# Performance work log

Measured on AMD Instinct MI355X. Metric: run time of the kernel, lower is better.

Reference implementation:

```python
import jax, jax.numpy as jnp
import numpy as np

S = 64        # FARGAN_SUBFRAME_SIZE
NSUB = 4      # FARGAN_SUBFRAMES
HOP = 256     # HOPSIZE = NSUB * S
NF = 256      # num_features
GC = 256      # global_channels
IC = NF + GC  # input_channels
B = 64
T = 100

NOISE_KEY = jax.random.key(1)


def _w(k, shape):
    return jax.random.normal(k, shape, dtype=jnp.float32) / np.sqrt(shape[-1]).astype(np.float32)


def setup_inputs() -> dict:
    key = jax.random.key(0)
    ks = jax.random.split(key, 20)
    return {
        'features': jax.random.normal(ks[0], (B, NF, T), dtype=jnp.float32),
        'global_features': jax.random.normal(ks[1], (B, GC, 1), dtype=jnp.float32),
        'in_W1': _w(ks[2], (IC, IC)),
        'in_b1': jnp.zeros((IC,), jnp.float32),
        'in_W2': _w(ks[3], (HOP, IC)),
        'in_b2': jnp.zeros((HOP,), jnp.float32),
        'fw_W': _w(ks[4], (S, 2 * S)),
        'fw_glu_W': _w(ks[5], (S, S)),
        'gru1_Wih': _w(ks[6], (3 * S, 2 * S)),
        'gru1_Whh': _w(ks[7], (3 * S, S)),
        'glu1_W': _w(ks[8], (S, S)),
        'gru2_Wih': _w(ks[9], (3 * S, 2 * S)),
        'gru2_Whh': _w(ks[10], (3 * S, S)),
        'glu2_W': _w(ks[11], (S, S)),
        'gru3_Wih': _w(ks[12], (3 * S, 2 * S)),
        'gru3_Whh': _w(ks[13], (3 * S, S)),
        'glu3_W': _w(ks[14], (S, S)),
        'skip_dense_W': _w(ks[15], (2 * S, 5 * S)),
        'skip_glu_W': _w(ks[16], (2 * S, 2 * S)),
        'out_W': _w(ks[17], (S, 2 * S)),
    }


def _noise(x, k):
    return jnp.clip(x + (jax.random.uniform(k, x.shape, x.dtype) - 0.5) * (1.0 / 127.0), -1.0, 1.0)


def _glu(x, W):
    return x * jax.nn.sigmoid(x @ W.T)


def _gru_cell(x, h, Wih, Whh):
    gi = x @ Wih.T  # [B, 3S]
    gh = h @ Whh.T
    i_r, i_z, i_n = jnp.split(gi, 3, axis=-1)
    h_r, h_z, h_n = jnp.split(gh, 3, axis=-1)
    r = jax.nn.sigmoid(i_r + h_r)
    z = jax.nn.sigmoid(i_z + h_z)
    n = jnp.tanh(i_n + r * h_n)
    return (1.0 - z) * n + z * h


def _forward(features, global_features, in_W1, in_b1, in_W2, in_b2, fw_W, fw_glu_W,
             gru1_Wih, gru1_Whh, glu1_W, gru2_Wih, gru2_Whh, glu2_W,
             gru3_Wih, gru3_Whh, glu3_W, skip_dense_W, skip_glu_W, out_W):
    b = features.shape[0]
    t = features.shape[2]
    g = global_features[:, :, 0]  # [B, GC]

    def subframe_step(sub, prev, st, key):
        h1, h2, h3, s3 = st
        kk = jax.random.split(key, 10)
        sub = _noise(sub, kk[0])
        prev = _noise(prev, kk[1])
        fw = _noise(_glu(jnp.tanh(jnp.concatenate([sub, s3], -1) @ fw_W.T), fw_glu_W), kk[2])
        h1n = _gru_cell(jnp.concatenate([fw, prev], -1), h1, gru1_Wih, gru1_Whh)
        g1 = _noise(_glu(_noise(h1n, kk[3]), glu1_W), kk[4])
        h2n = _gru_cell(jnp.concatenate([g1, prev], -1), h2, gru2_Wih, gru2_Whh)
        g2 = _noise(_glu(_noise(h2n, kk[5]), glu2_W), kk[6])
        h3n = _gru_cell(jnp.concatenate([g2, prev], -1), h3, gru3_Wih, gru3_Whh)
        g3 = _noise(_glu(_noise(h3n, kk[7]), glu3_W), kk[8])
        skip_feats = jnp.concatenate([g1, g2, g3, fw, prev], -1)  # [B, 5S]
        skip = _glu(_noise(jnp.tanh(skip_feats @ skip_dense_W.T), kk[9]), skip_glu_W)
        out = jnp.tanh(skip @ out_W.T)  # [B, S]
        return out, (h1n, h2n, h3n, sub)

    def frame_step(carry, f_t):
        st, prev, i = carry
        x = jnp.tanh(jnp.concatenate([f_t, g], -1) @ in_W1.T + in_b1) @ in_W2.T + in_b2  # [B, HOP]
        outs = []
        for s in range(NSUB):
            k = jax.random.fold_in(NOISE_KEY, i * NSUB + s)
            o, st = subframe_step(x[:, s * S:(s + 1) * S], prev, st, k)
            prev = o
            outs.append(o)
        return (st, prev, i + 1), jnp.concatenate(outs, -1)

    z = jnp.zeros((b, S), features.dtype)
    init = ((z, z, z, z), z, jnp.int32(0))
    xs = jnp.transpose(features, (2, 0, 1))  # [T, B, NF]
    _, ys = jax.lax.scan(frame_step, init, xs)  # [T, B, HOP]
    signal = jnp.transpose(ys, (1, 0, 2)).reshape(b, t * HOP)
    return signal[:, None, :]  # [B, 1, T*HOP]


def reference(features, global_features, in_W1, in_b1, in_W2, in_b2, fw_W, fw_glu_W,
              gru1_Wih, gru1_Whh, glu1_W, gru2_Wih, gru2_Whh, glu2_W,
              gru3_Wih, gru3_Whh, glu3_W, skip_dense_W, skip_glu_W, out_W):
    return _forward(features, global_features, in_W1, in_b1, in_W2, in_b2, fw_W, fw_glu_W,
                    gru1_Wih, gru1_Whh, glu1_W, gru2_Wih, gru2_Whh, glu2_W,
                    gru3_Wih, gru3_Whh, glu3_W, skip_dense_W, skip_glu_W, out_W)
```

## Files before the change

### kernel.cpp

```cpp
#include <hip/hip_runtime.h>
#include <stdint.h>

#define SS 64
#define BB 64
#define TT 100
#define HOPC 256
#define NFC 256
#define GCC 256
#define ICC 512
#define NC (1.0f/127.0f)
#define NBLK 64
#define NTHR 512

#define OFF_FW     0
#define OFF_FWGLU  8192
#define OFF_G1IH   12288
#define OFF_G1HH   36864
#define OFF_GLU1   49152
#define OFF_G2IH   53248
#define OFF_G2HH   77824
#define OFF_GLU2   90112
#define OFF_G3IH   94208
#define OFF_G3HH   118784
#define OFF_GLU3   131072
#define OFF_SKIPD  135168
#define OFF_SKIPG  176128
#define OFF_OUT    192512
#define W_TOTAL    200704
#define XALL_F32   (TT * BB * HOPC)

typedef _Float16 f16;
typedef _Float16 h2 __attribute__((ext_vector_type(2)));
union U16 { uint4 u; h2 h[4]; };

#if __has_builtin(__builtin_amdgcn_fdot2)
#define FDOT2(a, b, c) __builtin_amdgcn_fdot2((a), (b), (c), false)
#else
#define FDOT2(a, b, c) ((c) + (float)(a)[0] * (float)(b)[0] + (float)(a)[1] * (float)(b)[1])
#endif

__device__ __forceinline__ uint32_t rotl32(uint32_t x, int r) {
    return (x << r) | (x >> (32 - r));
}

__device__ __forceinline__ void tf2x32(uint32_t k0, uint32_t k1, uint32_t c0, uint32_t c1,
                                       uint32_t& o0, uint32_t& o1) {
    uint32_t k2 = k0 ^ k1 ^ 0x1BD11BDAu;
    uint32_t x0 = c0 + k0, x1 = c1 + k1;
    x0 += x1; x1 = rotl32(x1, 13); x1 ^= x0;
    x0 += x1; x1 = rotl32(x1, 15); x1 ^= x0;
    x0 += x1; x1 = rotl32(x1, 26); x1 ^= x0;
    x0 += x1; x1 = rotl32(x1, 6);  x1 ^= x0;
    x0 += k1; x1 += k2 + 1u;
    x0 += x1; x1 = rotl32(x1, 17); x1 ^= x0;
    x0 += x1; x1 = rotl32(x1, 29); x1 ^= x0;
    x0 += x1; x1 = rotl32(x1, 16); x1 ^= x0;
    x0 += x1; x1 = rotl32(x1, 24); x1 ^= x0;
    x0 += k2; x1 += k0 + 2u;
    x0 += x1; x1 = rotl32(x1, 13); x1 ^= x0;
    x0 += x1; x1 = rotl32(x1, 15); x1 ^= x0;
    x0 += x1; x1 = rotl32(x1, 26); x1 ^= x0;
    x0 += x1; x1 = rotl32(x1, 6);  x1 ^= x0;
    x0 += k0; x1 += k1 + 3u;
    x0 += x1; x1 = rotl32(x1, 17); x1 ^= x0;
    x0 += x1; x1 = rotl32(x1, 29); x1 ^= x0;
    x0 += x1; x1 = rotl32(x1, 16); x1 ^= x0;
    x0 += x1; x1 = rotl32(x1, 24); x1 ^= x0;
    x0 += k1; x1 += k2 + 4u;
    x0 += x1; x1 = rotl32(x1, 13); x1 ^= x0;
    x0 += x1; x1 = rotl32(x1, 15); x1 ^= x0;
    x0 += x1; x1 = rotl32(x1, 26); x1 ^= x0;
    x0 += x1; x1 = rotl32(x1, 6);  x1 ^= x0;
    x0 += k2; x1 += k0 + 5u;
    o0 = x0; o1 = x1;
}

__device__ __forceinline__ float unifP(uint32_t k0, uint32_t k1, uint32_t m) {
    uint32_t o0, o1;
    tf2x32(k0, k1, 0u, m, o0, o1);
    uint32_t bits = o0 ^ o1;
    return __uint_as_float((bits >> 9) | 0x3f800000u) - 1.0f;
}

__device__ __forceinline__ float clipf(float v) { return fminf(1.0f, fmaxf(-1.0f, v)); }
__device__ __forceinline__ float noiseu(float v, float u) {
    return clipf(v + (u - 0.5f) * NC);
}
__device__ __forceinline__ float sigmf(float v) {
    return __fdividef(1.0f, 1.0f + __expf(-v));
}
__device__ __forceinline__ float tanhfast(float x) {
    float ax = fminf(fabsf(x), 15.0f);
    float e = __expf(2.0f * ax);
    float r = __fdividef(e - 1.0f, e + 1.0f);
    return copysignf(r, x);
}

__device__ __forceinline__ float red8dpp(float v) {
    int t;
    t = __builtin_amdgcn_update_dpp(0, __float_as_int(v), 0xB1, 0xF, 0xF, true);
    v += __int_as_float(t);
    t = __builtin_amdgcn_update_dpp(0, __float_as_int(v), 0x4E, 0xF, 0xF, true);
    v += __int_as_float(t);
    t = __builtin_amdgcn_update_dpp(0, __float_as_int(v), 0x141, 0xF, 0xF, true);
    v += __int_as_float(t);
    return v;
}

__device__ __forceinline__ float dotU(const U16& w, const U16& x, float acc) {
#pragma unroll
    for (int i = 0; i < 4; ++i) acc = FDOT2(w.h[i], x.h[i], acc);
    return acc;
}

struct WF1  { U16 w[2]; };
struct WGRU { U16 wih[6]; U16 whh[3]; U16 glu; };
struct WSK  { U16 w[10]; };
struct WSG  { U16 w[4]; };

__device__ __forceinline__ void ldF1(const f16* W, int row, int g, WF1& r) {
    const f16* p = W + row * 128 + g * 16;
    r.w[0].u = *(const uint4*)p;
    r.w[1].u = *(const uint4*)(p + 8);
}
__device__ __forceinline__ void ldF2(const f16* W, int row, int g, U16& r) {
    r.u = *(const uint4*)(W + row * 64 + g * 8);
}
__device__ __forceinline__ void ldGRU(const f16* Wih, const f16* Whh, const f16* Glu,
                                      int row, int g, WGRU& r) {
#pragma unroll
    for (int j = 0; j < 3; ++j) {
        const f16* p = Wih + (row + 64 * j) * 128 + g * 16;
        r.wih[2 * j].u     = *(const uint4*)p;
        r.wih[2 * j + 1].u = *(const uint4*)(p + 8);
        r.whh[j].u = *(const uint4*)(Whh + (row + 64 * j) * 64 + g * 8);
    }
    r.glu.u = *(const uint4*)(Glu + row * 64 + g * 8);
}
__device__ __forceinline__ void ldSK(const f16* W, int row, int g, WSK& r) {
#pragma unroll
    for (int j = 0; j < 2; ++j) {
        const f16* p = W + (row + 64 * j) * 320 + g * 40;
#pragma unroll
        for (int i = 0; i < 5; ++i) r.w[5 * j + i].u = *(const uint4*)(p + 8 * i);
    }
}
__device__ __forceinline__ void ldSG(const f16* W, int row, int g, WSG& r) {
#pragma unroll
    for (int j = 0; j < 2; ++j) {
        const f16* p = W + (row + 64 * j) * 128 + g * 16;
        r.w[2 * j].u     = *(const uint4*)p;
        r.w[2 * j + 1].u = *(const uint4*)(p + 8);
    }
}

__device__ __forceinline__ void pinU(U16& r) {
    asm volatile("" : "+v"(r.u.x), "+v"(r.u.y), "+v"(r.u.z), "+v"(r.u.w));
}

struct SrcW { const float* p[14]; };

__global__ __launch_bounds__(256) void fargan_cvtw(SrcW s, f16* __restrict__ dst) {
    const int offs[15] = {0, 8192, 12288, 36864, 49152, 53248, 77824, 90112,
                          94208, 118784, 131072, 135168, 176128, 192512, 200704};
    int i = blockIdx.x * 256 + threadIdx.x;
    if (i >= W_TOTAL) return;
    int sgi = 0;
#pragma unroll
    for (int t = 1; t < 14; ++t) sgi += (i >= offs[t]);
    dst[i] = (f16)s.p[sgi][i - offs[sgi]];
}

__global__ __launch_bounds__(256) void fargan_tr(const float* __restrict__ f,
                                                 float* __restrict__ fT) {
    __shared__ float L[64][104];
    int b = blockIdx.x >> 2, c0 = (blockIdx.x & 3) * 64;
    for (int e = threadIdx.x; e < 6400; e += 256) {
        int r = e / 100, col = e - r * 100;
        L[r][col] = f[b * NFC * TT + (c0 + r) * TT + col];
    }
    __syncthreads();
    for (int e = threadIdx.x; e < 6400; e += 256) {
        int t = e >> 6, c = e & 63;
        fT[(t * BB + b) * NFC + c0 + c] = L[c][t];
    }
}

__global__ __launch_bounds__(256) void fargan_frame(
    const float* __restrict__ fT, const float* __restrict__ gfeat,
    const float* __restrict__ W1, const float* __restrict__ ib1,
    const float* __restrict__ W2, const float* __restrict__ ib2,
    float* __restrict__ xall)
{
    __shared__ __align__(16) float cat[16][ICC];
    __shared__ __align__(16) float zb[16][ICC];
    const int tid = threadIdx.x;
    const int t = blockIdx.x >> 2;
    const int q = blockIdx.x & 3;

    for (int bb = 0; bb < 16; ++bb) {
        int b = q * 16 + bb;
        for (int c = tid; c < ICC; c += 256) {
            float v = (c < NFC) ? fT[(t * BB + b) * NFC + c]
                                : gfeat[b * GCC + (c - NFC)];
            cat[bb][c] = v;
        }
    }
    __syncthreads();

    {
        int rg = tid & 63, bg = tid >> 6;
        int n0 = rg * 8, bb0 = bg * 4;
        float acc[8][4];
#pragma unroll
        for (int r = 0; r < 8; ++r)
#pragma unroll
            for (int j = 0; j < 4; ++j) acc[r][j] = 0.f;
        for (int k = 0; k < ICC; k += 4) {
            float4 cv[4];
#pragma unroll
            for (int j = 0; j < 4; ++j) cv[j] = *(const float4*)&cat[bb0 + j][k];
#pragma unroll
            for (int r = 0; r < 8; ++r) {
                float4 wv = *(const float4*)&W1[(n0 + r) * ICC + k];
#pragma unroll
                for (int j = 0; j < 4; ++j)
                    acc[r][j] += wv.x * cv[j].x + wv.y * cv[j].y + wv.z * cv[j].z + wv.w * cv[j].w;
            }
        }
#pragma unroll
        for (int r = 0; r < 8; ++r) {
            float bias = ib1[n0 + r];
#pragma unroll
            for (int j = 0; j < 4; ++j)
                zb[bb0 + j][n0 + r] = tanhf(acc[r][j] + bias);
        }
    }
    __syncthreads();

    {
        int rg = tid & 63, bg = tid >> 6;
        int n0 = rg * 4, bb0 = bg * 4;
        float acc[4][4];
#pragma unroll
        for (int r = 0; r < 4; ++r)
#pragma unroll
            for (int j = 0; j < 4; ++j) acc[r][j] = 0.f;
        for (int k = 0; k < ICC; k += 4) {
            float4 cv[4];
#pragma unroll
            for (int j = 0; j < 4; ++j) cv[j] = *(const float4*)&zb[bb0 + j][k];
#pragma unroll
            for (int r = 0; r < 4; ++r) {
                float4 wv = *(const float4*)&W2[(n0 + r) * ICC + k];
#pragma unroll
                for (int j = 0; j < 4; ++j)
                    acc[r][j] += wv.x * cv[j].x + wv.y * cv[j].y + wv.z * cv[j].z + wv.w * cv[j].w;
            }
        }
#pragma unroll
        for (int r = 0; r < 4; ++r) {
            float bias = ib2[n0 + r];
#pragma unroll
            for (int j = 0; j < 4; ++j) {
                int b = q * 16 + bb0 + j;
                xall[(t * BB + b) * HOPC + n0 + r] = acc[r][j] + bias;
            }
        }
    }
}

__global__ __launch_bounds__(512, 2) void fargan_seq(
    const float* __restrict__ xall, const f16* __restrict__ wh,
    float* __restrict__ outp)
{
    const int tid = threadIdx.x;
    const int row = tid >> 3;
    const int g = tid & 7;
    const int bg = blockIdx.x;

    __shared__ __align__(16) f16 XH[128];
    __shared__ __align__(16) f16 SKXH[320];
    __shared__ __align__(16) f16 TWH[64], HNH[64];
    __shared__ __align__(16) f16 SPNH[128], SKVH[128];
    __shared__ __align__(16) f16 HH[2][3][64];
    __shared__ __align__(16) float Hf[2][3][64];
    __shared__ __align__(16) float UNF[704];
    __shared__ uint32_t kkb[2][20];

    WF1 rF1;  ldF1(wh + OFF_FW, row, g, rF1);
    U16 rF2;  ldF2(wh + OFF_FWGLU, row, g, rF2);
    WGRU rG1; ldGRU(wh + OFF_G1IH, wh + OFF_G1HH, wh + OFF_GLU1, row, g, rG1);
    WGRU rG2; ldGRU(wh + OFF_G2IH, wh + OFF_G2HH, wh + OFF_GLU2, row, g, rG2);
    WGRU rG3; ldGRU(wh + OFF_G3IH, wh + OFF_G3HH, wh + OFF_GLU3, row, g, rG3);
    WSG rSG;  ldSG(wh + OFF_SKIPG, row, g, rSG);
    WF1 rOUT; ldF1(wh + OFF_OUT, row, g, rOUT);

    pinU(rF1.w[0]); pinU(rF1.w[1]); pinU(rF2);
#pragma unroll
    for (int j = 0; j < 6; ++j) { pinU(rG1.wih[j]); pinU(rG2.wih[j]); pinU(rG3.wih[j]); }
#pragma unroll
    for (int j = 0; j < 3; ++j) { pinU(rG1.whh[j]); pinU(rG2.whh[j]); pinU(rG3.whh[j]); }
    pinU(rG1.glu); pinU(rG2.glu); pinU(rG3.glu);
#pragma unroll
    for (int j = 0; j < 4; ++j) pinU(rSG.w[j]);
    pinU(rOUT.w[0]); pinU(rOUT.w[1]);

    float prevO = 0.f, xs_old = 0.f;
    if (g == 0) {
#pragma unroll
        for (int i = 0; i < 3; ++i) { Hf[0][i][row] = 0.f; HH[0][i][row] = (f16)0.f; }
        XH[row] = (f16)0.f; XH[64 + row] = (f16)0.f;
    }
    if (tid < 10) {
        uint32_t f0, f1; tf2x32(0u, 1u, 0u, 0u, f0, f1);
        uint32_t A, Bv;  tf2x32(f0, f1, 0u, (uint32_t)tid, A, Bv);
        kkb[0][2 * tid] = A; kkb[0][2 * tid + 1] = Bv;
    }
    __syncthreads();

    for (int t = 0; t < TT; ++t) {
        for (int s = 0; s < 4; ++s) {
            const int idx = t * 4 + s;
            const int p = idx & 1;

            float xv = xall[(t * BB + bg) * HOPC + s * SS + row];
            if (g == 0) {
                const uint32_t m64 = (uint32_t)(bg * 64 + row);
                float u0 = unifP(kkb[p][0], kkb[p][1], m64);
                float u1 = unifP(kkb[p][2], kkb[p][3], m64);
                float xs = noiseu(xv, u0);
                XH[row] = (f16)xs; XH[64 + row] = (f16)xs_old; xs_old = xs;
                SKXH[256 + row] = (f16)noiseu(prevO, u1);
            } else {
                int wid = row * 7 + g - 1;
                int j = 128 + wid;
                int sl = j >> 6;
                UNF[j] = unifP(kkb[p][2 * sl], kkb[p][2 * sl + 1],
                               (uint32_t)(bg * 64 + (j & 63)));
                if (wid < 128)
                    UNF[576 + wid] = unifP(kkb[p][18], kkb[p][19],
                                           (uint32_t)(bg * 128 + wid));
            }
            if (g == 7 && row >= 54) {
                int i = row - 54;
                uint32_t f0, f1; tf2x32(0u, 1u, 0u, (uint32_t)(idx + 1), f0, f1);
                uint32_t A, Bv;  tf2x32(f0, f1, 0u, (uint32_t)i, A, Bv);
                kkb[p ^ 1][2 * i] = A; kkb[p ^ 1][2 * i + 1] = Bv;
            }
            __syncthreads();

            float twv;
            {
                U16 xa, xb;
                xa.u = *(const uint4*)&XH[g * 16];
                xb.u = *(const uint4*)&XH[g * 16 + 8];
                float a = dotU(rF1.w[0], xa, 0.f);
                a = dotU(rF1.w[1], xb, a);
                twv = tanhfast(red8dpp(a));
                if (g == 0) TWH[row] = (f16)twv;
            }
            __syncthreads();

            {
                U16 xa; xa.u = *(const uint4*)&TWH[g * 8];
                float a = red8dpp(dotU(rF2, xa, 0.f));
                if (g == 0) SKXH[192 + row] = (f16)noiseu(twv * sigmf(a), UNF[128 + row]);
            }
            __syncthreads();

#define GRU_STEP(RG, XPTR, GI, UH, UG, GOFF)                                               \
            {                                                                               \
                const f16* xin = (XPTR);                                                    \
                U16 xa, xb, xh;                                                             \
                xa.u = *(const uint4*)xin;                                                  \
                xb.u = *(const uint4*)(xin + 8);                                            \
                xh.u = *(const uint4*)&HH[p][GI][g * 8];                                    \
                float ai0 = 0, ai1 = 0, ai2 = 0, ah0 = 0, ah1 = 0, ah2 = 0;                 \
                ai0 = dotU(RG.wih[0], xa, ai0); ai0 = dotU(RG.wih[1], xb, ai0);             \
                ai1 = dotU(RG.wih[2], xa, ai1); ai1 = dotU(RG.wih[3], xb, ai1);             \
                ai2 = dotU(RG.wih[4], xa, ai2); ai2 = dotU(RG.wih[5], xb, ai2);             \
                ah0 = dotU(RG.whh[0], xh, ah0);                                             \
                ah1 = dotU(RG.whh[1], xh, ah1);                                             \
                ah2 = dotU(RG.whh[2], xh, ah2);                                             \
                ai0 = red8dpp(ai0); ai1 = red8dpp(ai1); ai2 = red8dpp(ai2);                 \
                ah0 = red8dpp(ah0); ah1 = red8dpp(ah1); ah2 = red8dpp(ah2);                 \
                float hold = Hf[p][GI][row];                                                \
                float r  = sigmf(ai0 + ah0);                                                \
                float z  = sigmf(ai1 + ah1);                                                \
                float nn = tanhfast(ai2 + r * ah2);                                         \
                float hnew = (1.f - z) * nn + z * hold;                                     \
                float hNv = noiseu(hnew, UNF[(UH) + row]);                                  \
                if (g == 0) {                                                               \
                    Hf[p ^ 1][GI][row] = hnew;                                              \
                    HH[p ^ 1][GI][row] = (f16)hnew;                                         \
                    HNH[row] = (f16)hNv;                                                    \
                }                                                                           \
                __syncthreads();                                                            \
                U16 xg; xg.u = *(const uint4*)&HNH[g * 8];                                  \
                float ag = red8dpp(dotU(RG.glu, xg, 0.f));                                  \
                if (g == 0) SKXH[(GOFF) + row] =                                            \
                    (f16)noiseu(hNv * sigmf(ag), UNF[(UG) + row]);                          \
            }                                                                               \
            __syncthreads();

            GRU_STEP(rG1, SKXH + 192 + g * 16, 0, 192, 256, 0)
            GRU_STEP(rG2, (g < 4 ? SKXH + g * 16 : SKXH + 256 + (g - 4) * 16), 1, 320, 384, 64)
            WSK rSK; ldSK(wh + OFF_SKIPD, row, g, rSK);
            GRU_STEP(rG3, (g < 4 ? SKXH + 64 + g * 16 : SKXH + 256 + (g - 4) * 16), 2, 448, 512, 128)
#undef GRU_STEP

            float sp0, sp1;
            {
                U16 xs[5];
#pragma unroll
                for (int i = 0; i < 5; ++i) xs[i].u = *(const uint4*)&SKXH[g * 40 + 8 * i];
                float a0 = 0, a1 = 0;
#pragma unroll
                for (int i = 0; i < 5; ++i) {
                    a0 = dotU(rSK.w[i], xs[i], a0);
                    a1 = dotU(rSK.w[5 + i], xs[i], a1);
                }
                sp0 = noiseu(tanhfast(red8dpp(a0)), UNF[576 + row]);
                sp1 = noiseu(tanhfast(red8dpp(a1)), UNF[640 + row]);
                if (g == 0) { SPNH[row] = (f16)sp0; SPNH[64 + row] = (f16)sp1; }
            }
            __syncthreads();

            {
                U16 xa, xb;
                xa.u = *(const uint4*)&SPNH[g * 16];
                xb.u = *(const uint4*)&SPNH[g * 16 + 8];
                float a0 = dotU(rSG.w[0], xa, 0.f); a0 = dotU(rSG.w[1], xb, a0);
                float a1 = dotU(rSG.w[2], xa, 0.f); a1 = dotU(rSG.w[3], xb, a1);
                a0 = red8dpp(a0); a1 = red8dpp(a1);
                if (g == 0) {
                    SKVH[row]      = (f16)(sp0 * sigmf(a0));
                    SKVH[64 + row] = (f16)(sp1 * sigmf(a1));
                }
            }
            __syncthreads();

            {
                U16 xa, xb;
                xa.u = *(const uint4*)&SKVH[g * 16];
                xb.u = *(const uint4*)&SKVH[g * 16 + 8];
                float a = dotU(rOUT.w[0], xa, 0.f);
                a = dotU(rOUT.w[1], xb, a);
                float o = tanhfast(red8dpp(a));
                prevO = o;
                if (g == 0) outp[bg * (TT * HOPC) + t * HOPC + s * SS + row] = o;
            }
        }
    }
}

extern "C" void kernel_launch(void* const* d_in, const int* in_sizes, int n_in,
                              void* d_out, int out_size, void* d_ws, size_t ws_size,
                              hipStream_t stream) {
    const float* features = (const float*)d_in[0];
    const float* gfeat    = (const float*)d_in[1];
    const float* W1       = (const float*)d_in[2];
    const float* ib1      = (const float*)d_in[3];
    const float* W2       = (const float*)d_in[4];
    const float* ib2      = (const float*)d_in[5];

    float* xall = (float*)d_ws;
    float* fT   = xall + XALL_F32;
    f16*   wh   = (f16*)(fT + XALL_F32);
    float* outp = (float*)d_out;

    SrcW sw;
    for (int i = 0; i < 14; ++i) sw.p[i] = (const float*)d_in[6 + i];

    hipLaunchKernelGGL(fargan_cvtw, dim3((W_TOTAL + 255) / 256), dim3(256), 0, stream, sw, wh);
    hipLaunchKernelGGL(fargan_tr, dim3(256), dim3(256), 0, stream, features, fT);
    hipLaunchKernelGGL(fargan_frame, dim3(TT * 4), dim3(256), 0, stream,
                       fT, gfeat, W1, ib1, W2, ib2, xall);
    hipLaunchKernelGGL(fargan_seq, dim3(NBLK), dim3(NTHR), 0, stream, xall, wh, outp);
}
```

Measured before the change: 2.834 ms.

## Precompute RNG keys, double-buffer noise generation, prefetch inputs, lighten barriers

All 401 per-subframe Threefry keys are computed once at kernel start into a shared table, so the serial per-step key derivation is gone. Uniform noise for the next subframe is generated into a double-buffered array, with the work split across the idle slots of several stages. Next-frame input values are prefetched into registers a frame ahead. __syncthreads is replaced by an inline-asm LDS wait plus s_barrier, which skips waiting on global memory; this relies on no cross-thread dependence through global memory and uses more shared memory.

```diff
diff --git a/kernel.cpp b/kernel.cpp
--- a/kernel.cpp
+++ b/kernel.cpp
@@ -96,6 +96,10 @@
     return copysignf(r, x);
 }
 
+__device__ __forceinline__ void bar_lds() {
+    asm volatile("s_waitcnt lgkmcnt(0)\n\ts_barrier" ::: "memory");
+}
+
 __device__ __forceinline__ float red8dpp(float v) {
     int t;
     t = __builtin_amdgcn_update_dpp(0, __float_as_int(v), 0xB1, 0xF, 0xF, true);
@@ -285,8 +289,8 @@
     __shared__ __align__(16) f16 SPNH[128], SKVH[128];
     __shared__ __align__(16) f16 HH[2][3][64];
     __shared__ __align__(16) float Hf[2][3][64];
-    __shared__ __align__(16) float UNF[704];
-    __shared__ uint32_t kkb[2][20];
+    __shared__ __align__(16) float UNF[2][704];
+    __shared__ uint32_t KK[401][20];
 
     WF1 rF1;  ldF1(wh + OFF_FW, row, g, rF1);
     U16 rF2;  ldF2(wh + OFF_FWGLU, row, g, rF2);
@@ -312,43 +316,49 @@
         for (int i = 0; i < 3; ++i) { Hf[0][i][row] = 0.f; HH[0][i][row] = (f16)0.f; }
         XH[row] = (f16)0.f; XH[64 + row] = (f16)0.f;
     }
-    if (tid < 10) {
-        uint32_t f0, f1; tf2x32(0u, 1u, 0u, 0u, f0, f1);
-        uint32_t A, Bv;  tf2x32(f0, f1, 0u, (uint32_t)tid, A, Bv);
-        kkb[0][2 * tid] = A; kkb[0][2 * tid + 1] = Bv;
+
+    for (int e = tid; e < 4010; e += NTHR) {
+        int ii = e / 10, ki = e - ii * 10;
+        uint32_t f0, f1; tf2x32(0u, 1u, 0u, (uint32_t)ii, f0, f1);
+        uint32_t A, Bv;  tf2x32(f0, f1, 0u, (uint32_t)ki, A, Bv);
+        KK[ii][2 * ki] = A; KK[ii][2 * ki + 1] = Bv;
     }
     __syncthreads();
 
+    for (int j = tid; j < 704; j += NTHR) {
+        int sl = j >> 6;
+        int kx = (sl < 9) ? 2 * sl : 18;
+        uint32_t m = (sl < 9) ? (uint32_t)(bg * 64 + (j & 63))
+                              : (uint32_t)(bg * 128 + (j - 576));
+        UNF[0][j] = unifP(KK[0][kx], KK[0][kx + 1], m);
+    }
+
+    float xf0 = xall[(0 * BB + bg) * HOPC + 0 * SS + row];
+    float xf1 = xall[(0 * BB + bg) * HOPC + 1 * SS + row];
+    float xf2 = xall[(0 * BB + bg) * HOPC + 2 * SS + row];
+    float xf3 = xall[(0 * BB + bg) * HOPC + 3 * SS + row];
+    __syncthreads();
+
     for (int t = 0; t < TT; ++t) {
+        const int tn = (t + 1 < TT) ? t + 1 : t;
+        float xn0 = xall[(tn * BB + bg) * HOPC + 0 * SS + row];
+        float xn1 = xall[(tn * BB + bg) * HOPC + 1 * SS + row];
+        float xn2 = xall[(tn * BB + bg) * HOPC + 2 * SS + row];
+        float xn3 = xall[(tn * BB + bg) * HOPC + 3 * SS + row];
+
         for (int s = 0; s < 4; ++s) {
             const int idx = t * 4 + s;
             const int p = idx & 1;
 
-            float xv = xall[(t * BB + bg) * HOPC + s * SS + row];
             if (g == 0) {
-                const uint32_t m64 = (uint32_t)(bg * 64 + row);
-                float u0 = unifP(kkb[p][0], kkb[p][1], m64);
-                float u1 = unifP(kkb[p][2], kkb[p][3], m64);
+                float u0 = UNF[p][row];
+                float u1 = UNF[p][64 + row];
+                float xv = (s == 0) ? xf0 : (s == 1) ? xf1 : (s == 2) ? xf2 : xf3;
                 float xs = noiseu(xv, u0);
                 XH[row] = (f16)xs; XH[64 + row] = (f16)xs_old; xs_old = xs;
                 SKXH[256 + row] = (f16)noiseu(prevO, u1);
-            } else {
-                int wid = row * 7 + g - 1;
-                int j = 128 + wid;
-                int sl = j >> 6;
-                UNF[j] = unifP(kkb[p][2 * sl], kkb[p][2 * sl + 1],
-                               (uint32_t)(bg * 64 + (j & 63)));
-                if (wid < 128)
-                    UNF[576 + wid] = unifP(kkb[p][18], kkb[p][19],
-                                           (uint32_t)(bg * 128 + wid));
-            }
-            if (g == 7 && row >= 54) {
-                int i = row - 54;
-                uint32_t f0, f1; tf2x32(0u, 1u, 0u, (uint32_t)(idx + 1), f0, f1);
-                uint32_t A, Bv;  tf2x32(f0, f1, 0u, (uint32_t)i, A, Bv);
-                kkb[p ^ 1][2 * i] = A; kkb[p ^ 1][2 * i + 1] = Bv;
-            }
-            __syncthreads();
+            }
+            bar_lds();
 
             float twv;
             {
@@ -360,22 +370,28 @@
                 twv = tanhfast(red8dpp(a));
                 if (g == 0) TWH[row] = (f16)twv;
             }
-            __syncthreads();
+            bar_lds();
 
             {
                 U16 xa; xa.u = *(const uint4*)&TWH[g * 8];
+                if (tid < 256) {
+                    int kx = 2 * (tid >> 6);
+                    UNF[p ^ 1][tid] = unifP(KK[idx + 1][kx], KK[idx + 1][kx + 1],
+                                            (uint32_t)(bg * 64 + (tid & 63)));
+                }
                 float a = red8dpp(dotU(rF2, xa, 0.f));
-                if (g == 0) SKXH[192 + row] = (f16)noiseu(twv * sigmf(a), UNF[128 + row]);
-            }
-            __syncthreads();
-
-#define GRU_STEP(RG, XPTR, GI, UH, UG, GOFF)                                               \
+                if (g == 0) SKXH[192 + row] = (f16)noiseu(twv * sigmf(a), UNF[p][128 + row]);
+            }
+            bar_lds();
+
+#define GRU_STEP(RG, XPTR, GI, UH, UG, GOFF, EXTRA)                                         \
             {                                                                               \
                 const f16* xin = (XPTR);                                                    \
                 U16 xa, xb, xh;                                                             \
                 xa.u = *(const uint4*)xin;                                                  \
                 xb.u = *(const uint4*)(xin + 8);                                            \
                 xh.u = *(const uint4*)&HH[p][GI][g * 8];                                    \
+                EXTRA;                                                                      \
                 float ai0 = 0, ai1 = 0, ai2 = 0, ah0 = 0, ah1 = 0, ah2 = 0;                 \
                 ai0 = dotU(RG.wih[0], xa, ai0); ai0 = dotU(RG.wih[1], xb, ai0);             \
                 ai1 = dotU(RG.wih[2], xa, ai1); ai1 = dotU(RG.wih[3], xb, ai1);             \
@@ -390,25 +406,37 @@
                 float z  = sigmf(ai1 + ah1);                                                \
                 float nn = tanhfast(ai2 + r * ah2);                                         \
                 float hnew = (1.f - z) * nn + z * hold;                                     \
-                float hNv = noiseu(hnew, UNF[(UH) + row]);                                  \
+                float hNv = noiseu(hnew, UNF[p][(UH) + row]);                               \
                 if (g == 0) {                                                               \
                     Hf[p ^ 1][GI][row] = hnew;                                              \
                     HH[p ^ 1][GI][row] = (f16)hnew;                                         \
                     HNH[row] = (f16)hNv;                                                    \
                 }                                                                           \
-                __syncthreads();                                                            \
+                bar_lds();                                                                  \
                 U16 xg; xg.u = *(const uint4*)&HNH[g * 8];                                  \
                 float ag = red8dpp(dotU(RG.glu, xg, 0.f));                                  \
                 if (g == 0) SKXH[(GOFF) + row] =                                            \
-                    (f16)noiseu(hNv * sigmf(ag), UNF[(UG) + row]);                          \
+                    (f16)noiseu(hNv * sigmf(ag), UNF[p][(UG) + row]);                       \
             }                                                                               \
-            __syncthreads();
-
-            GRU_STEP(rG1, SKXH + 192 + g * 16, 0, 192, 256, 0)
-            GRU_STEP(rG2, (g < 4 ? SKXH + g * 16 : SKXH + 256 + (g - 4) * 16), 1, 320, 384, 64)
+            bar_lds();
+
+#define NOISE_A2 do { if (tid >= 256) {                                                     \
+                int kx = 2 * (tid >> 6);                                                    \
+                UNF[p ^ 1][tid] = unifP(KK[idx + 1][kx], KK[idx + 1][kx + 1],               \
+                                        (uint32_t)(bg * 64 + (tid & 63))); } } while (0)
+#define NOISE_B do { int j2 = tid + 512; if (j2 < 704) {                                    \
+                int kx = (j2 < 576) ? 16 : 18;                                              \
+                uint32_t m2 = (j2 < 576) ? (uint32_t)(bg * 64 + (j2 & 63))                  \
+                                         : (uint32_t)(bg * 128 + (j2 - 576));               \
+                UNF[p ^ 1][j2] = unifP(KK[idx + 1][kx], KK[idx + 1][kx + 1], m2); } } while (0)
+
+            GRU_STEP(rG1, SKXH + 192 + g * 16, 0, 192, 256, 0, NOISE_A2)
+            GRU_STEP(rG2, (g < 4 ? SKXH + g * 16 : SKXH + 256 + (g - 4) * 16), 1, 320, 384, 64, NOISE_B)
             WSK rSK; ldSK(wh + OFF_SKIPD, row, g, rSK);
-            GRU_STEP(rG3, (g < 4 ? SKXH + 64 + g * 16 : SKXH + 256 + (g - 4) * 16), 2, 448, 512, 128)
+            GRU_STEP(rG3, (g < 4 ? SKXH + 64 + g * 16 : SKXH + 256 + (g - 4) * 16), 2, 448, 512, 128, ((void)0))
 #undef GRU_STEP
+#undef NOISE_A2
+#undef NOISE_B
 
             float sp0, sp1;
             {
@@ -421,11 +449,11 @@
                     a0 = dotU(rSK.w[i], xs[i], a0);
                     a1 = dotU(rSK.w[5 + i], xs[i], a1);
                 }
-                sp0 = noiseu(tanhfast(red8dpp(a0)), UNF[576 + row]);
-                sp1 = noiseu(tanhfast(red8dpp(a1)), UNF[640 + row]);
+                sp0 = noiseu(tanhfast(red8dpp(a0)), UNF[p][576 + row]);
+                sp1 = noiseu(tanhfast(red8dpp(a1)), UNF[p][640 + row]);
                 if (g == 0) { SPNH[row] = (f16)sp0; SPNH[64 + row] = (f16)sp1; }
             }
-            __syncthreads();
+            bar_lds();
 
             {
                 U16 xa, xb;
@@ -439,7 +467,7 @@
                     SKVH[64 + row] = (f16)(sp1 * sigmf(a1));
                 }
             }
-            __syncthreads();
+            bar_lds();
 
             {
                 U16 xa, xb;
@@ -452,6 +480,7 @@
                 if (g == 0) outp[bg * (TT * HOPC) + t * HOPC + s * SS + row] = o;
             }
         }
+        xf0 = xn0; xf1 = xn1; xf2 = xn2; xf3 = xn3;
     }
 }
 
```

Result: faster. 2.701 ms (-4.7%).

## Process four batch rows per block and pipeline noise generation across steps

Applied to the files above, without the earlier changes.

Each block of the sequential kernel now handles four batch elements instead of one, so every barrier and register-resident weight load is amortized over four independent recurrences. The uniform noise for the next subframe is precomputed into a double-buffered LDS array, spread across the compute phases, and the key schedule runs two steps ahead. __syncthreads is replaced by a plain LDS waitcnt plus s_barrier. The grid drops to 16 blocks, so far fewer CUs are used and each block runs longer, more serialized work; register pressure also rises with the per-chain arrays.

```diff
diff --git a/kernel.cpp b/kernel.cpp
--- a/kernel.cpp
+++ b/kernel.cpp
@@ -9,7 +9,8 @@
 #define GCC 256
 #define ICC 512
 #define NC (1.0f/127.0f)
-#define NBLK 64
+#define CH 4
+#define NBLK (64/CH)
 #define NTHR 512
 
 #define OFF_FW     0
@@ -96,6 +97,10 @@
     return copysignf(r, x);
 }
 
+__device__ __forceinline__ void bar_lds() {
+    asm volatile("s_waitcnt lgkmcnt(0)\n\ts_barrier" ::: "memory");
+}
+
 __device__ __forceinline__ float red8dpp(float v) {
     int t;
     t = __builtin_amdgcn_update_dpp(0, __float_as_int(v), 0xB1, 0xF, 0xF, true);
@@ -279,13 +284,13 @@
     const int g = tid & 7;
     const int bg = blockIdx.x;
 
-    __shared__ __align__(16) f16 XH[128];
-    __shared__ __align__(16) f16 SKXH[320];
-    __shared__ __align__(16) f16 TWH[64], HNH[64];
-    __shared__ __align__(16) f16 SPNH[128], SKVH[128];
-    __shared__ __align__(16) f16 HH[2][3][64];
-    __shared__ __align__(16) float Hf[2][3][64];
-    __shared__ __align__(16) float UNF[704];
+    __shared__ __align__(16) f16 XH[CH][128];
+    __shared__ __align__(16) f16 SKXH[CH][320];
+    __shared__ __align__(16) f16 TWH[CH][64], HNH[CH][64];
+    __shared__ __align__(16) f16 SPNH[CH][128], SKVH[CH][128];
+    __shared__ __align__(16) f16 HH[2][CH][3][64];
+    __shared__ __align__(16) float Hf[2][CH][3][64];
+    __shared__ __align__(16) float UNF[2][CH][704];
     __shared__ uint32_t kkb[2][20];
 
     WF1 rF1;  ldF1(wh + OFF_FW, row, g, rF1);
@@ -306,153 +311,215 @@
     for (int j = 0; j < 4; ++j) pinU(rSG.w[j]);
     pinU(rOUT.w[0]); pinU(rOUT.w[1]);
 
-    float prevO = 0.f, xs_old = 0.f;
-    if (g == 0) {
-#pragma unroll
-        for (int i = 0; i < 3; ++i) { Hf[0][i][row] = 0.f; HH[0][i][row] = (f16)0.f; }
-        XH[row] = (f16)0.f; XH[64 + row] = (f16)0.f;
+    float prevO[CH], xs_old[CH];
+#pragma unroll
+    for (int c = 0; c < CH; ++c) { prevO[c] = 0.f; xs_old[c] = 0.f; }
+
+    if (tid < 256) {
+        int c = tid >> 6, r = tid & 63;
+#pragma unroll
+        for (int i = 0; i < 3; ++i) { Hf[0][c][i][r] = 0.f; HH[0][c][i][r] = (f16)0.f; }
+        XH[c][r] = (f16)0.f; XH[c][64 + r] = (f16)0.f;
     }
     if (tid < 10) {
         uint32_t f0, f1; tf2x32(0u, 1u, 0u, 0u, f0, f1);
         uint32_t A, Bv;  tf2x32(f0, f1, 0u, (uint32_t)tid, A, Bv);
         kkb[0][2 * tid] = A; kkb[0][2 * tid + 1] = Bv;
+    } else if (tid >= 32 && tid < 42) {
+        int i = tid - 32;
+        uint32_t f0, f1; tf2x32(0u, 1u, 0u, 1u, f0, f1);
+        uint32_t A, Bv;  tf2x32(f0, f1, 0u, (uint32_t)i, A, Bv);
+        kkb[1][2 * i] = A; kkb[1][2 * i + 1] = Bv;
     }
     __syncthreads();
+
+    for (int e = tid; e < CH * 704; e += NTHR) {
+        int c2 = (e >= 2112) ? 3 : (e >= 1408) ? 2 : (e >= 704) ? 1 : 0;
+        int j2 = e - c2 * 704;
+        int sl = j2 >> 6;
+        int kx = (sl < 9) ? 2 * sl : 18;
+        uint32_t m2 = (sl < 9) ? (uint32_t)((bg * CH + c2) * 64 + (j2 & 63))
+                               : (uint32_t)((bg * CH + c2) * 128 + (j2 - 576));
+        UNF[0][c2][j2] = unifP(kkb[0][kx], kkb[0][kx + 1], m2);
+    }
+    __syncthreads();
+
+#define GEN_SITE(SITEI) do {                                                    \
+        int id_ = (SITEI) * 512 + tid;                                          \
+        if (id_ < CH * 704) {                                                   \
+            int c2 = (id_ >= 2112) ? 3 : (id_ >= 1408) ? 2 : (id_ >= 704) ? 1 : 0; \
+            int j2 = id_ - c2 * 704;                                            \
+            int sl = j2 >> 6;                                                   \
+            int kx = (sl < 9) ? 2 * sl : 18;                                    \
+            uint32_t m2 = (sl < 9) ? (uint32_t)((bg * CH + c2) * 64 + (j2 & 63))   \
+                                   : (uint32_t)((bg * CH + c2) * 128 + (j2 - 576)); \
+            UNF[p ^ 1][c2][j2] = unifP(kkb[p ^ 1][kx], kkb[p ^ 1][kx + 1], m2); \
+        } } while (0)
 
     for (int t = 0; t < TT; ++t) {
         for (int s = 0; s < 4; ++s) {
             const int idx = t * 4 + s;
             const int p = idx & 1;
 
-            float xv = xall[(t * BB + bg) * HOPC + s * SS + row];
-            if (g == 0) {
-                const uint32_t m64 = (uint32_t)(bg * 64 + row);
-                float u0 = unifP(kkb[p][0], kkb[p][1], m64);
-                float u1 = unifP(kkb[p][2], kkb[p][3], m64);
-                float xs = noiseu(xv, u0);
-                XH[row] = (f16)xs; XH[64 + row] = (f16)xs_old; xs_old = xs;
-                SKXH[256 + row] = (f16)noiseu(prevO, u1);
-            } else {
-                int wid = row * 7 + g - 1;
-                int j = 128 + wid;
-                int sl = j >> 6;
-                UNF[j] = unifP(kkb[p][2 * sl], kkb[p][2 * sl + 1],
-                               (uint32_t)(bg * 64 + (j & 63)));
-                if (wid < 128)
-                    UNF[576 + wid] = unifP(kkb[p][18], kkb[p][19],
-                                           (uint32_t)(bg * 128 + wid));
-            }
             if (g == 7 && row >= 54) {
                 int i = row - 54;
-                uint32_t f0, f1; tf2x32(0u, 1u, 0u, (uint32_t)(idx + 1), f0, f1);
+                uint32_t f0, f1; tf2x32(0u, 1u, 0u, (uint32_t)(idx + 2), f0, f1);
                 uint32_t A, Bv;  tf2x32(f0, f1, 0u, (uint32_t)i, A, Bv);
-                kkb[p ^ 1][2 * i] = A; kkb[p ^ 1][2 * i + 1] = Bv;
-            }
-            __syncthreads();
-
-            float twv;
-            {
+                kkb[p][2 * i] = A; kkb[p][2 * i + 1] = Bv;
+            }
+            if (g == 0) {
+#pragma unroll
+                for (int c = 0; c < CH; ++c) {
+                    float xv = xall[(t * BB + (bg * CH + c)) * HOPC + s * SS + row];
+                    float u0 = UNF[p][c][row];
+                    float u1 = UNF[p][c][64 + row];
+                    float xs = noiseu(xv, u0);
+                    XH[c][row] = (f16)xs; XH[c][64 + row] = (f16)xs_old[c]; xs_old[c] = xs;
+                    SKXH[c][256 + row] = (f16)noiseu(prevO[c], u1);
+                }
+            }
+            bar_lds();
+
+            float twv[CH];
+#pragma unroll
+            for (int c = 0; c < CH; ++c) {
                 U16 xa, xb;
-                xa.u = *(const uint4*)&XH[g * 16];
-                xb.u = *(const uint4*)&XH[g * 16 + 8];
+                xa.u = *(const uint4*)&XH[c][g * 16];
+                xb.u = *(const uint4*)&XH[c][g * 16 + 8];
                 float a = dotU(rF1.w[0], xa, 0.f);
                 a = dotU(rF1.w[1], xb, a);
-                twv = tanhfast(red8dpp(a));
-                if (g == 0) TWH[row] = (f16)twv;
-            }
-            __syncthreads();
+                twv[c] = tanhfast(red8dpp(a));
+                if (g == 0) TWH[c][row] = (f16)twv[c];
+            }
+            bar_lds();
 
             {
-                U16 xa; xa.u = *(const uint4*)&TWH[g * 8];
-                float a = red8dpp(dotU(rF2, xa, 0.f));
-                if (g == 0) SKXH[192 + row] = (f16)noiseu(twv * sigmf(a), UNF[128 + row]);
-            }
-            __syncthreads();
-
-#define GRU_STEP(RG, XPTR, GI, UH, UG, GOFF)                                               \
+                U16 xa[CH];
+#pragma unroll
+                for (int c = 0; c < CH; ++c) xa[c].u = *(const uint4*)&TWH[c][g * 8];
+                GEN_SITE(0);
+#pragma unroll
+                for (int c = 0; c < CH; ++c) {
+                    float a = red8dpp(dotU(rF2, xa[c], 0.f));
+                    if (g == 0) SKXH[c][192 + row] =
+                        (f16)noiseu(twv[c] * sigmf(a), UNF[p][c][128 + row]);
+                }
+            }
+            bar_lds();
+
+#define GRU_STEP(RG, XEXPR, GI, UH, UG, GOFF, PRE1, PRE2)                                   \
             {                                                                               \
-                const f16* xin = (XPTR);                                                    \
-                U16 xa, xb, xh;                                                             \
-                xa.u = *(const uint4*)xin;                                                  \
-                xb.u = *(const uint4*)(xin + 8);                                            \
-                xh.u = *(const uint4*)&HH[p][GI][g * 8];                                    \
-                float ai0 = 0, ai1 = 0, ai2 = 0, ah0 = 0, ah1 = 0, ah2 = 0;                 \
-                ai0 = dotU(RG.wih[0], xa, ai0); ai0 = dotU(RG.wih[1], xb, ai0);             \
-                ai1 = dotU(RG.wih[2], xa, ai1); ai1 = dotU(RG.wih[3], xb, ai1);             \
-                ai2 = dotU(RG.wih[4], xa, ai2); ai2 = dotU(RG.wih[5], xb, ai2);             \
-                ah0 = dotU(RG.whh[0], xh, ah0);                                             \
-                ah1 = dotU(RG.whh[1], xh, ah1);                                             \
-                ah2 = dotU(RG.whh[2], xh, ah2);                                             \
-                ai0 = red8dpp(ai0); ai1 = red8dpp(ai1); ai2 = red8dpp(ai2);                 \
-                ah0 = red8dpp(ah0); ah1 = red8dpp(ah1); ah2 = red8dpp(ah2);                 \
-                float hold = Hf[p][GI][row];                                                \
-                float r  = sigmf(ai0 + ah0);                                                \
-                float z  = sigmf(ai1 + ah1);                                                \
-                float nn = tanhfast(ai2 + r * ah2);                                         \
-                float hnew = (1.f - z) * nn + z * hold;                                     \
-                float hNv = noiseu(hnew, UNF[(UH) + row]);                                  \
-                if (g == 0) {                                                               \
-                    Hf[p ^ 1][GI][row] = hnew;                                              \
-                    HH[p ^ 1][GI][row] = (f16)hnew;                                         \
-                    HNH[row] = (f16)hNv;                                                    \
+                float hNv[CH];                                                              \
+                U16 xa[CH], xb[CH], xh[CH];                                                 \
+                _Pragma("unroll")                                                           \
+                for (int c = 0; c < CH; ++c) {                                              \
+                    const f16* xin = (XEXPR);                                               \
+                    xa[c].u = *(const uint4*)xin;                                           \
+                    xb[c].u = *(const uint4*)(xin + 8);                                     \
+                    xh[c].u = *(const uint4*)&HH[p][c][GI][g * 8];                          \
                 }                                                                           \
-                __syncthreads();                                                            \
-                U16 xg; xg.u = *(const uint4*)&HNH[g * 8];                                  \
-                float ag = red8dpp(dotU(RG.glu, xg, 0.f));                                  \
-                if (g == 0) SKXH[(GOFF) + row] =                                            \
-                    (f16)noiseu(hNv * sigmf(ag), UNF[(UG) + row]);                          \
+                PRE1;                                                                       \
+                _Pragma("unroll")                                                           \
+                for (int c = 0; c < CH; ++c) {                                              \
+                    float ai0 = 0, ai1 = 0, ai2 = 0, ah0 = 0, ah1 = 0, ah2 = 0;             \
+                    ai0 = dotU(RG.wih[0], xa[c], ai0); ai0 = dotU(RG.wih[1], xb[c], ai0);   \
+                    ai1 = dotU(RG.wih[2], xa[c], ai1); ai1 = dotU(RG.wih[3], xb[c], ai1);   \
+                    ai2 = dotU(RG.wih[4], xa[c], ai2); ai2 = dotU(RG.wih[5], xb[c], ai2);   \
+                    ah0 = dotU(RG.whh[0], xh[c], ah0);                                      \
+                    ah1 = dotU(RG.whh[1], xh[c], ah1);                                      \
+                    ah2 = dotU(RG.whh[2], xh[c], ah2);                                      \
+                    ai0 = red8dpp(ai0); ai1 = red8dpp(ai1); ai2 = red8dpp(ai2);             \
+                    ah0 = red8dpp(ah0); ah1 = red8dpp(ah1); ah2 = red8dpp(ah2);             \
+                    float hold = Hf[p][c][GI][row];                                         \
+                    float r  = sigmf(ai0 + ah0);                                            \
+                    float z  = sigmf(ai1 + ah1);                                            \
+                    float nn = tanhfast(ai2 + r * ah2);                                     \
+                    float hnew = (1.f - z) * nn + z * hold;                                 \
+                    hNv[c] = noiseu(hnew, UNF[p][c][(UH) + row]);                           \
+                    if (g == 0) {                                                           \
+                        Hf[p ^ 1][c][GI][row] = hnew;                                       \
+                        HH[p ^ 1][c][GI][row] = (f16)hnew;                                  \
+                        HNH[c][row] = (f16)hNv[c];                                          \
+                    }                                                                       \
+                }                                                                           \
+                bar_lds();                                                                  \
+                PRE2;                                                                       \
+                _Pragma("unroll")                                                           \
+                for (int c = 0; c < CH; ++c) {                                              \
+                    U16 xg; xg.u = *(const uint4*)&HNH[c][g * 8];                           \
+                    float ag = red8dpp(dotU(RG.glu, xg, 0.f));                              \
+                    if (g == 0) SKXH[c][(GOFF) + row] =                                     \
+                        (f16)noiseu(hNv[c] * sigmf(ag), UNF[p][c][(UG) + row]);             \
+                }                                                                           \
             }                                                                               \
-            __syncthreads();
-
-            GRU_STEP(rG1, SKXH + 192 + g * 16, 0, 192, 256, 0)
-            GRU_STEP(rG2, (g < 4 ? SKXH + g * 16 : SKXH + 256 + (g - 4) * 16), 1, 320, 384, 64)
-            WSK rSK; ldSK(wh + OFF_SKIPD, row, g, rSK);
-            GRU_STEP(rG3, (g < 4 ? SKXH + 64 + g * 16 : SKXH + 256 + (g - 4) * 16), 2, 448, 512, 128)
+            bar_lds();
+
+            WSK rSK;
+            GRU_STEP(rG1, &SKXH[c][192 + g * 16], 0, 192, 256, 0,
+                     GEN_SITE(1), (void)0)
+            GRU_STEP(rG2, (g < 4 ? &SKXH[c][g * 16] : &SKXH[c][256 + (g - 4) * 16]),
+                     1, 320, 384, 64, GEN_SITE(2), (void)0)
+            GRU_STEP(rG3, (g < 4 ? &SKXH[c][64 + g * 16] : &SKXH[c][256 + (g - 4) * 16]),
+                     2, 448, 512, 128, GEN_SITE(3),
+                     ldSK(wh + OFF_SKIPD, row, g, rSK))
 #undef GRU_STEP
 
-            float sp0, sp1;
+            float sp0[CH], sp1[CH];
             {
-                U16 xs[5];
-#pragma unroll
-                for (int i = 0; i < 5; ++i) xs[i].u = *(const uint4*)&SKXH[g * 40 + 8 * i];
-                float a0 = 0, a1 = 0;
-#pragma unroll
-                for (int i = 0; i < 5; ++i) {
-                    a0 = dotU(rSK.w[i], xs[i], a0);
-                    a1 = dotU(rSK.w[5 + i], xs[i], a1);
+                GEN_SITE(4);
+#pragma unroll
+                for (int c = 0; c < CH; ++c) {
+                    U16 xs5[5];
+#pragma unroll
+                    for (int i = 0; i < 5; ++i) xs5[i].u = *(const uint4*)&SKXH[c][g * 40 + 8 * i];
+                    float a0 = 0, a1 = 0;
+#pragma unroll
+                    for (int i = 0; i < 5; ++i) {
+                        a0 = dotU(rSK.w[i], xs5[i], a0);
+                        a1 = dotU(rSK.w[5 + i], xs5[i], a1);
+                    }
+                    sp0[c] = noiseu(tanhfast(red8dpp(a0)), UNF[p][c][576 + row]);
+                    sp1[c] = noiseu(tanhfast(red8dpp(a1)), UNF[p][c][640 + row]);
+                    if (g == 0) { SPNH[c][row] = (f16)sp0[c]; SPNH[c][64 + row] = (f16)sp1[c]; }
                 }
-                sp0 = noiseu(tanhfast(red8dpp(a0)), UNF[576 + row]);
-                sp1 = noiseu(tanhfast(red8dpp(a1)), UNF[640 + row]);
-                if (g == 0) { SPNH[row] = (f16)sp0; SPNH[64 + row] = (f16)sp1; }
-            }
-            __syncthreads();
+            }
+            bar_lds();
 
             {
-                U16 xa, xb;
-                xa.u = *(const uint4*)&SPNH[g * 16];
-                xb.u = *(const uint4*)&SPNH[g * 16 + 8];
-                float a0 = dotU(rSG.w[0], xa, 0.f); a0 = dotU(rSG.w[1], xb, a0);
-                float a1 = dotU(rSG.w[2], xa, 0.f); a1 = dotU(rSG.w[3], xb, a1);
-                a0 = red8dpp(a0); a1 = red8dpp(a1);
-                if (g == 0) {
-                    SKVH[row]      = (f16)(sp0 * sigmf(a0));
-                    SKVH[64 + row] = (f16)(sp1 * sigmf(a1));
+                GEN_SITE(5);
+#pragma unroll
+                for (int c = 0; c < CH; ++c) {
+                    U16 xa, xb;
+                    xa.u = *(const uint4*)&SPNH[c][g * 16];
+                    xb.u = *(const uint4*)&SPNH[c][g * 16 + 8];
+                    float a0 = dotU(rSG.w[0], xa, 0.f); a0 = dotU(rSG.w[1], xb, a0);
+                    float a1 = dotU(rSG.w[2], xa, 0.f); a1 = dotU(rSG.w[3], xb, a1);
+                    a0 = red8dpp(a0); a1 = red8dpp(a1);
+                    if (g == 0) {
+                        SKVH[c][row]      = (f16)(sp0[c] * sigmf(a0));
+                        SKVH[c][64 + row] = (f16)(sp1[c] * sigmf(a1));
+                    }
                 }
             }
-            __syncthreads();
+            bar_lds();
 
             {
-                U16 xa, xb;
-                xa.u = *(const uint4*)&SKVH[g * 16];
-                xb.u = *(const uint4*)&SKVH[g * 16 + 8];
-                float a = dotU(rOUT.w[0], xa, 0.f);
-                a = dotU(rOUT.w[1], xb, a);
-                float o = tanhfast(red8dpp(a));
-                prevO = o;
-                if (g == 0) outp[bg * (TT * HOPC) + t * HOPC + s * SS + row] = o;
+#pragma unroll
+                for (int c = 0; c < CH; ++c) {
+                    U16 xa, xb;
+                    xa.u = *(const uint4*)&SKVH[c][g * 16];
+                    xb.u = *(const uint4*)&SKVH[c][g * 16 + 8];
+                    float a = dotU(rOUT.w[0], xa, 0.f);
+                    a = dotU(rOUT.w[1], xb, a);
+                    float o = tanhfast(red8dpp(a));
+                    prevO[c] = o;
+                    if (g == 0)
+                        outp[(bg * CH + c) * (TT * HOPC) + t * HOPC + s * SS + row] = o;
+                }
             }
         }
     }
+#undef GEN_SITE
 }
 
 extern "C" void kernel_launch(void* const* d_in, const int* in_sizes, int n_in,
```

Measured after the change: 7.506 ms. +164.9%, slower.
